# Performance work log

Hardware: AMD Instinct MI355X
Metric: run time of the kernel (lower is better)

The kernel has to match this reference:

```python
import jax, jax.numpy as jnp
import numpy as np

N, E, G = 100000, 500000, 1000


def _gat(h_in, src, dst, W, a_s, a_d, b, n):
    # PyG GATConv, heads=1, concat=True, negative_slope=0.2, self-loops already in src/dst
    h = h_in @ W.T                                  # [N, out]
    alpha_src = h @ a_s                             # [N]
    alpha_dst = h @ a_d                             # [N]
    e = jax.nn.leaky_relu(alpha_src[src] + alpha_dst[dst], 0.2)  # [E']
    m = jax.ops.segment_max(e, dst, num_segments=n)
    ex = jnp.exp(e - m[dst])
    den = jax.ops.segment_sum(ex, dst, num_segments=n)
    alpha = ex / den[dst]                           # segment softmax over incoming edges
    out = jax.ops.segment_sum(h[src] * alpha[:, None], dst, num_segments=n)
    return out + b


def _forward(x, edge_index, batch, w1, b1, w2, b2, w3, b3,
             g1w, g1as, g1ad, g1b, g2w, g2as, g2ad, g2b,
             g3w, g3as, g3ad, g3b, g4w, g4as, g4ad, g4b,
             g5w, g5as, g5ad, g5b, lw, lb):
    n = x.shape[0]
    h = jax.nn.relu(x @ w1.T + b1)
    h = jax.nn.relu(h @ w2.T + b2)
    h = jax.nn.relu(h @ w3.T + b3)
    loops = jnp.arange(n)
    src = jnp.concatenate([edge_index[0], loops])   # add self-loops
    dst = jnp.concatenate([edge_index[1], loops])
    h = jax.nn.relu(_gat(h, src, dst, g1w, g1as, g1ad, g1b, n))
    h = jax.nn.relu(_gat(h, src, dst, g2w, g2as, g2ad, g2b, n))
    h = jax.nn.relu(_gat(h, src, dst, g3w, g3as, g3ad, g3b, n))
    h = jax.nn.relu(_gat(h, src, dst, g4w, g4as, g4ad, g4b, n))
    h = jax.nn.relu(_gat(h, src, dst, g5w, g5as, g5ad, g5b, n))
    sums = jax.ops.segment_sum(h, batch, num_segments=G)            # [G,32]
    cnt = jax.ops.segment_sum(jnp.ones((n,), h.dtype), batch, num_segments=G)
    mean = sums / jnp.maximum(cnt, 1.0)[:, None]
    return jax.nn.sigmoid(mean @ lw.T + lb)         # [G,1]


def setup_inputs() -> dict:
    key = jax.random.key(0)
    ks = jax.random.split(key, 24)

    def lin(k, o, i):
        k1, k2 = jax.random.split(k)
        s = 1.0 / np.sqrt(i)
        return (jax.random.uniform(k1, (o, i), jnp.float32, -s, s),
                jax.random.uniform(k2, (o,), jnp.float32, -s, s))

    def gat_p(k, i, o):
        k1, k2, k3 = jax.random.split(k, 3)
        s = 1.0 / np.sqrt(i)
        W = jax.random.uniform(k1, (o, i), jnp.float32, -s, s)
        a_s = jax.random.normal(k2, (o,), jnp.float32) / np.sqrt(o)
        a_d = jax.random.normal(k3, (o,), jnp.float32) / np.sqrt(o)
        return W, a_s, a_d, jnp.zeros((o,), jnp.float32)

    inp = {}
    inp['x'] = jax.random.normal(ks[0], (N, 1), jnp.float32)
    inp['edge_index'] = jax.random.randint(ks[1], (2, E), 0, N)
    inp['batch'] = jnp.sort(jax.random.randint(ks[2], (N,), 0, G))
    inp['w1'], inp['b1'] = lin(ks[3], 16, 1)
    inp['w2'], inp['b2'] = lin(ks[4], 32, 16)
    inp['w3'], inp['b3'] = lin(ks[5], 64, 32)
    dims = [(64, 128), (128, 256), (256, 128), (128, 64), (64, 32)]
    for j, (i, o) in enumerate(dims, start=1):
        W, a_s, a_d, b = gat_p(ks[5 + j], i, o)
        inp[f'g{j}w'], inp[f'g{j}as'], inp[f'g{j}ad'], inp[f'g{j}b'] = W, a_s, a_d, b
    inp['lw'], inp['lb'] = lin(ks[12], 1, 32)
    return inp


def reference(x, edge_index, batch, w1, b1, w2, b2, w3, b3,
              g1w, g1as, g1ad, g1b, g2w, g2as, g2ad, g2b,
              g3w, g3as, g3ad, g3b, g4w, g4as, g4ad, g4b,
              g5w, g5as, g5ad, g5b, lw, lb):
    return _forward(x, edge_index, batch, w1, b1, w2, b2, w3, b3,
                    g1w, g1as, g1ad, g1b, g2w, g2as, g2ad, g2b,
                    g3w, g3as, g3ad, g3b, g4w, g4as, g4ad, g4b,
                    g5w, g5as, g5ad, g5b, lw, lb)
```

## Files before the change

kernel.cpp:

```cpp
#include <hip/hip_runtime.h>
#include <math.h>

typedef __attribute__((ext_vector_type(8))) __bf16 bf16x8;
typedef __attribute__((ext_vector_type(4))) float f32x4;

__device__ inline unsigned short f2bf(float f) {
    unsigned int i = __float_as_uint(f);
    unsigned int r = i + 0x7fffu + ((i >> 16) & 1u);
    return (unsigned short)(r >> 16);
}
__device__ inline float bf2f(unsigned short u) {
    return __uint_as_float(((unsigned int)u) << 16);
}

__global__ __launch_bounds__(256) void prelude_kernel(
    const float* __restrict__ x,
    const float* __restrict__ w1, const float* __restrict__ b1,
    const float* __restrict__ w2, const float* __restrict__ b2,
    const float* __restrict__ w3, const float* __restrict__ b3,
    unsigned short* __restrict__ h0, int n,
    const float* __restrict__ g0, const float* __restrict__ g1, const float* __restrict__ g2,
    const float* __restrict__ g3, const float* __restrict__ g4,
    unsigned short* __restrict__ wbAll,
    const int* __restrict__ batch, int* __restrict__ gstart, int G,
    const int* __restrict__ dst, int* __restrict__ deg, int E,
    int mlpB, int f2bfB, int gsB, int histB,
    const float* __restrict__ as1, const float* __restrict__ ad1,
    float* __restrict__ s1out, float* __restrict__ d1out,
    const float* __restrict__ as2, const float* __restrict__ ad2,
    float* __restrict__ pv2) {
    int b = blockIdx.x;
    int tid = threadIdx.x;
    if (b < mlpB) {
        __shared__ float4 sw1q[4], sb1q[4];
        __shared__ float4 sw2q[128];
        __shared__ float4 sw3q[512];
        __shared__ float2 psd1[64];
        __shared__ float sb2l[32], sb3l[64];
        __shared__ float pres[4][64], predu[4][64];
        {
            int ii = tid & 63, ch = tid >> 6;
            const float* gp = g0 + (size_t)(ch * 32) * 64 + ii;
            float s = 0.f, d = 0.f;
#pragma unroll 4
            for (int o = 0; o < 32; o++) {
                float w = gp[o * 64];
                s += as1[ch * 32 + o] * w;
                d += ad1[ch * 32 + o] * w;
            }
            pres[ch][ii] = s;
            predu[ch][ii] = d;
        }
        if (tid < 4) { sw1q[tid] = ((const float4*)w1)[tid]; sb1q[tid] = ((const float4*)b1)[tid]; }
        if (tid >= 32 && tid < 64) sb2l[tid - 32] = b2[tid - 32];
        if (tid >= 64 && tid < 128) sb3l[tid - 64] = b3[tid - 64];
        for (int i = tid; i < 128; i += 256) sw2q[i] = ((const float4*)w2)[i];
        for (int i = tid; i < 512; i += 256) sw3q[i] = ((const float4*)w3)[i];
        __syncthreads();
        if (tid < 64) {
            psd1[tid] =
                make_float2(pres[0][tid] + pres[1][tid] + pres[2][tid] + pres[3][tid],
                            predu[0][tid] + predu[1][tid] + predu[2][tid] + predu[3][tid]);
        }
        __syncthreads();
        int node = b * 256 + tid;
        if (node >= n) return;
        float xv = x[node];
        float t1[16], t2[32];
#pragma unroll
        for (int q = 0; q < 4; q++) {
            float4 wv = sw1q[q], bv = sb1q[q];
            t1[q * 4 + 0] = fmaxf(wv.x * xv + bv.x, 0.f);
            t1[q * 4 + 1] = fmaxf(wv.y * xv + bv.y, 0.f);
            t1[q * 4 + 2] = fmaxf(wv.z * xv + bv.z, 0.f);
            t1[q * 4 + 3] = fmaxf(wv.w * xv + bv.w, 0.f);
        }
#pragma unroll
        for (int o = 0; o < 32; o++) {
            float a = sb2l[o];
#pragma unroll
            for (int q = 0; q < 4; q++) {
                float4 wv = sw2q[o * 4 + q];
                a += wv.x * t1[q * 4] + wv.y * t1[q * 4 + 1] + wv.z * t1[q * 4 + 2] +
                     wv.w * t1[q * 4 + 3];
            }
            t2[o] = fmaxf(a, 0.f);
        }
        float sdot = 0.f, ddot = 0.f;
        uint4* gp = (uint4*)(h0 + (size_t)node * 64);
#pragma unroll
        for (int c = 0; c < 8; c++) {
            unsigned int wvec[4];
#pragma unroll
            for (int p = 0; p < 4; p++) {
                int o = c * 8 + p * 2;
                float a0 = sb3l[o], a1 = sb3l[o + 1];
#pragma unroll
                for (int q = 0; q < 8; q++) {
                    float4 wa = sw3q[o * 8 + q];
                    float4 wb = sw3q[(o + 1) * 8 + q];
                    a0 += wa.x * t2[q * 4] + wa.y * t2[q * 4 + 1] + wa.z * t2[q * 4 + 2] +
                          wa.w * t2[q * 4 + 3];
                    a1 += wb.x * t2[q * 4] + wb.y * t2[q * 4 + 1] + wb.z * t2[q * 4 + 2] +
                          wb.w * t2[q * 4 + 3];
                }
                float r0 = fmaxf(a0, 0.f), r1 = fmaxf(a1, 0.f);
                float2 q0 = psd1[o], q1 = psd1[o + 1];
                sdot += r0 * q0.x + r1 * q1.x;
                ddot += r0 * q0.y + r1 * q1.y;
                wvec[p] = (unsigned)f2bf(r0) | ((unsigned)f2bf(r1) << 16);
            }
            gp[c] = make_uint4(wvec[0], wvec[1], wvec[2], wvec[3]);
        }
        s1out[node] = sdot;
        d1out[node] = ddot;
    } else if (b < mlpB + f2bfB) {
        int i = (b - mlpB) * 256 + tid;
        float v;
        if (i < 8192) v = g0[i];
        else if (i < 40960) v = g1[i - 8192];
        else if (i < 73728) v = g2[i - 40960];
        else if (i < 81920) v = g3[i - 73728];
        else if (i < 83968) v = g4[i - 81920];
        else return;
        wbAll[i] = f2bf(v);
    } else if (b < mlpB + f2bfB + gsB) {
        int g = (b - mlpB - f2bfB) * 256 + tid;
        if (g > G) return;
        if (g == G) { gstart[G] = n; return; }
        int lo = 0, hi = n;
        while (lo < hi) {
            int mid = (lo + hi) >> 1;
            if (batch[mid] < g) lo = mid + 1;
            else hi = mid;
        }
        gstart[g] = lo;
    } else if (b < mlpB + f2bfB + gsB + histB) {
        int e = (b - mlpB - f2bfB - gsB) * 256 + tid;
        if (e >= E + n) return;
        int d = (e < E) ? dst[e] : (e - E);
        atomicAdd(&deg[d], 1);
    } else {
        if (tid < 128) {
            float s = 0.f;
            for (int o = 0; o < 256; o++) s += as2[o] * g1[o * 128 + tid];
            pv2[tid] = s;
        } else {
            int c = tid - 128;
            float s = 0.f;
            for (int o = 0; o < 256; o++) s += ad2[o] * g1[o * 128 + c];
            pv2[128 + c] = s;
        }
    }
}

template <int BN, int EPI>
__global__ __launch_bounds__(256) void gemm_mfma(
    const unsigned short* __restrict__ A, const unsigned short* __restrict__ Wb,
    unsigned short* __restrict__ Cb,
    const float* __restrict__ avs, const float* __restrict__ avd,
    float* __restrict__ as_, float* __restrict__ ad_,
    const float* __restrict__ bias, int n, int K, int O) {
    constexpr int SN = BN / 32;
    __shared__ unsigned short As[128][72];
    __shared__ unsigned short Ws[BN][72];
    int tid = threadIdx.x;
    int row0 = blockIdx.x * 128, col0 = blockIdx.y * BN;
    int w = tid >> 6, lane = tid & 63;
    int wr = w >> 1, wc = w & 1;
    int quad = lane >> 4, l15 = lane & 15;
    f32x4 acc[4][SN];
#pragma unroll
    for (int mi = 0; mi < 4; mi++)
#pragma unroll
        for (int ni = 0; ni < SN; ni++) acc[mi][ni] = (f32x4){0.f, 0.f, 0.f, 0.f};

    for (int k0 = 0; k0 < K; k0 += 64) {
#pragma unroll
        for (int i = tid; i < 1024; i += 256) {
            int r = i >> 3, c8 = i & 7;
            int gr = row0 + r;
            uint4 v = make_uint4(0u, 0u, 0u, 0u);
            if (gr < n) v = *(const uint4*)(A + (size_t)gr * K + k0 + c8 * 8);
            *(uint4*)&As[r][c8 * 8] = v;
        }
#pragma unroll
        for (int i = tid; i < BN * 8; i += 256) {
            int r = i >> 3, c8 = i & 7;
            uint4 v = *(const uint4*)(Wb + (size_t)(col0 + r) * K + k0 + c8 * 8);
            *(uint4*)&Ws[r][c8 * 8] = v;
        }
        __syncthreads();
#pragma unroll
        for (int kk = 0; kk < 64; kk += 32) {
            bf16x8 bfr[SN];
#pragma unroll
            for (int ni = 0; ni < SN; ni++)
                bfr[ni] = *(const bf16x8*)&Ws[wc * (BN / 2) + ni * 16 + l15][kk + quad * 8];
#pragma unroll
            for (int mi = 0; mi < 4; mi++) {
                bf16x8 afr = *(const bf16x8*)&As[wr * 64 + mi * 16 + l15][kk + quad * 8];
#pragma unroll
                for (int ni = 0; ni < SN; ni++)
                    acc[mi][ni] = __builtin_amdgcn_mfma_f32_16x16x32_bf16(afr, bfr[ni],
                                                                          acc[mi][ni], 0, 0, 0);
            }
        }
        __syncthreads();
    }
    float avsv[SN], avdv[SN], bv[SN];
    int gc[SN];
#pragma unroll
    for (int ni = 0; ni < SN; ni++) {
        gc[ni] = col0 + wc * (BN / 2) + ni * 16 + l15;
        if constexpr (EPI != 2) {
            avsv[ni] = avs[gc[ni]];
            avdv[ni] = avd[gc[ni]];
        }
        if constexpr (EPI >= 1) bv[ni] = bias[gc[ni]];
    }
#pragma unroll
    for (int mi = 0; mi < 4; mi++) {
        int gm0 = row0 + wr * 64 + mi * 16 + quad * 4;
        float ps[4] = {0.f, 0.f, 0.f, 0.f}, pd[4] = {0.f, 0.f, 0.f, 0.f};
#pragma unroll
        for (int ni = 0; ni < SN; ni++) {
#pragma unroll
            for (int r = 0; r < 4; r++) {
                float d = acc[mi][ni][r];
                if constexpr (EPI >= 1) d = fmaxf(d + bv[ni], 0.f);
                int gm = gm0 + r;
                if (gm < n) Cb[(size_t)gm * O + gc[ni]] = f2bf(d);
                if constexpr (EPI != 2) {
                    ps[r] += d * avsv[ni];
                    pd[r] += d * avdv[ni];
                }
            }
        }
        if constexpr (EPI != 2) {
#pragma unroll
            for (int r = 0; r < 4; r++) {
#pragma unroll
                for (int m = 1; m <= 8; m <<= 1) {
                    ps[r] += __shfl_xor(ps[r], m);
                    pd[r] += __shfl_xor(pd[r], m);
                }
            }
            if (l15 == 0) {
#pragma unroll
                for (int r = 0; r < 4; r++) {
                    int gm = gm0 + r;
                    if (gm < n) {
                        atomicAdd(&as_[gm], ps[r]);
                        atomicAdd(&ad_[gm], pd[r]);
                    }
                }
            }
        }
    }
}

__global__ void scan_block_sums(const int* __restrict__ deg, int* __restrict__ bsums, int n) {
    __shared__ int sdata[256];
    int tid = threadIdx.x;
    int base = blockIdx.x * 1024 + tid * 4;
    int s = 0;
    for (int i = 0; i < 4; i++) {
        int g = base + i;
        if (g < n) s += deg[g];
    }
    sdata[tid] = s;
    __syncthreads();
    for (int off = 128; off > 0; off >>= 1) {
        if (tid < off) sdata[tid] += sdata[tid + off];
        __syncthreads();
    }
    if (tid == 0) bsums[blockIdx.x] = sdata[0];
}

__global__ void scan_write(const int* __restrict__ deg, const int* __restrict__ bsums,
                           int* __restrict__ rowptr, int* __restrict__ cursor, int n, int nb) {
    __shared__ int sdata[256];
    int tid = threadIdx.x;
    sdata[tid] = (tid < blockIdx.x && tid < nb) ? bsums[tid] : 0;
    __syncthreads();
    for (int off = 128; off > 0; off >>= 1) {
        if (tid < off) sdata[tid] += sdata[tid + off];
        __syncthreads();
    }
    int base = sdata[0];
    __syncthreads();
    int gbase = blockIdx.x * 1024 + tid * 4;
    int v[4];
    int s = 0;
    for (int i = 0; i < 4; i++) {
        int g = gbase + i;
        v[i] = (g < n) ? deg[g] : 0;
        s += v[i];
    }
    sdata[tid] = s;
    __syncthreads();
    for (int off = 1; off < 256; off <<= 1) {
        int t = (tid >= off) ? sdata[tid - off] : 0;
        __syncthreads();
        sdata[tid] += t;
        __syncthreads();
    }
    int excl = sdata[tid] - s + base;
    for (int i = 0; i < 4; i++) {
        int g = gbase + i;
        if (g < n) { rowptr[g] = excl; cursor[g] = excl; }
        excl += v[i];
    }
    if (blockIdx.x == gridDim.x - 1 && tid == 255) rowptr[n] = base + sdata[255];
}

__global__ void scatter_kernel(const int* __restrict__ esrc_in, const int* __restrict__ edst_in,
                               int* __restrict__ cursor, int* __restrict__ esrc, int E, int n) {
    int e = blockIdx.x * 256 + threadIdx.x;
    if (e >= E + n) return;
    int s, d;
    if (e < E) { s = esrc_in[e]; d = edst_in[e]; }
    else { s = e - E; d = e - E; }
    int pos = atomicAdd(&cursor[d], 1);
    esrc[pos] = s;
}

template <int O, bool BIASRELU>
__global__ __launch_bounds__(256) void gat_aggregate(
    const unsigned short* __restrict__ hl, const float* __restrict__ as_,
    const float* __restrict__ ad_, const int* __restrict__ rowptr,
    const int* __restrict__ esrc, const float* __restrict__ bias,
    unsigned short* __restrict__ hout, int n, float* __restrict__ zeroBuf, int zeroCnt) {
    int gtid = blockIdx.x * 256 + threadIdx.x;
    if (gtid < zeroCnt) zeroBuf[gtid] = 0.f;
    constexpr int C8 = O / 8;
    constexpr int EPP = 16 / C8;
    int tid = threadIdx.x;
    int v = blockIdx.x * 16 + (tid >> 4);
    int l = tid & 15;
    int gbase = tid & 48;
    if (v >= n) return;
    int beg = rowptr[v], end = rowptr[v + 1];
    int deg = end - beg;
    float adv = ad_[v];
    int sub = l / C8;
    int c = l % C8;
    float acc[8] = {0.f, 0.f, 0.f, 0.f, 0.f, 0.f, 0.f, 0.f};
    if (deg <= 16) {
        int sreg = v;
        float e = -1e30f;
        if (l < deg) {
            sreg = esrc[beg + l];
            float t = as_[sreg] + adv;
            e = (t > 0.f) ? t : 0.2f * t;
        }
        float m = e;
#pragma unroll
        for (int o = 8; o > 0; o >>= 1) m = fmaxf(m, __shfl_xor(m, o));
        float ex = (l < deg) ? __expf(e - m) : 0.f;
        float sum = ex;
#pragma unroll
        for (int o = 8; o > 0; o >>= 1) sum += __shfl_xor(sum, o);
        float alpha_r = ex / sum;
        for (int j0 = 0; j0 < deg; j0 += EPP) {
            int idx = j0 + sub;
            int cidx = (idx < deg) ? idx : 0;
            float alpha = __shfl(alpha_r, gbase + cidx);
            int s2 = __shfl(sreg, gbase + cidx);
            if (idx >= deg) alpha = 0.f;
            uint4 raw = ((const uint4*)(hl + (size_t)s2 * O))[c];
            acc[0] += alpha * __uint_as_float(raw.x << 16);
            acc[1] += alpha * __uint_as_float(raw.x & 0xffff0000u);
            acc[2] += alpha * __uint_as_float(raw.y << 16);
            acc[3] += alpha * __uint_as_float(raw.y & 0xffff0000u);
            acc[4] += alpha * __uint_as_float(raw.z << 16);
            acc[5] += alpha * __uint_as_float(raw.z & 0xffff0000u);
            acc[6] += alpha * __uint_as_float(raw.w << 16);
            acc[7] += alpha * __uint_as_float(raw.w & 0xffff0000u);
        }
    } else {
        float mymax = -1e30f;
        for (int j = beg + l; j < end; j += 16) {
            float e = as_[esrc[j]] + adv;
            e = (e > 0.f) ? e : 0.2f * e;
            mymax = fmaxf(mymax, e);
        }
#pragma unroll
        for (int o = 8; o > 0; o >>= 1) mymax = fmaxf(mymax, __shfl_xor(mymax, o));
        float mysum = 0.f;
        for (int j = beg + l; j < end; j += 16) {
            float e = as_[esrc[j]] + adv;
            e = (e > 0.f) ? e : 0.2f * e;
            mysum += __expf(e - mymax);
        }
#pragma unroll
        for (int o = 8; o > 0; o >>= 1) mysum += __shfl_xor(mysum, o);
        float invden = 1.f / mysum;
        for (int j0 = beg; j0 < end; j0 += EPP) {
            int j = j0 + sub;
            bool valid = j < end;
            int s = valid ? esrc[j] : v;
            float e = as_[s] + adv;
            e = (e > 0.f) ? e : 0.2f * e;
            float alpha = valid ? __expf(e - mymax) * invden : 0.f;
            uint4 raw = ((const uint4*)(hl + (size_t)s * O))[c];
            acc[0] += alpha * __uint_as_float(raw.x << 16);
            acc[1] += alpha * __uint_as_float(raw.x & 0xffff0000u);
            acc[2] += alpha * __uint_as_float(raw.y << 16);
            acc[3] += alpha * __uint_as_float(raw.y & 0xffff0000u);
            acc[4] += alpha * __uint_as_float(raw.z << 16);
            acc[5] += alpha * __uint_as_float(raw.z & 0xffff0000u);
            acc[6] += alpha * __uint_as_float(raw.w << 16);
            acc[7] += alpha * __uint_as_float(raw.w & 0xffff0000u);
        }
    }
#pragma unroll
    for (int o = C8; o < 16; o <<= 1)
#pragma unroll
        for (int k = 0; k < 8; k++) acc[k] += __shfl_xor(acc[k], o);
    if (l < C8) {
        unsigned short ov[8];
#pragma unroll
        for (int k = 0; k < 8; k++) {
            float val = acc[k];
            if constexpr (BIASRELU) val = fmaxf(val + bias[c * 8 + k], 0.f);
            ov[k] = f2bf(val);
        }
        uint4 packed;
        packed.x = (unsigned)ov[0] | ((unsigned)ov[1] << 16);
        packed.y = (unsigned)ov[2] | ((unsigned)ov[3] << 16);
        packed.z = (unsigned)ov[4] | ((unsigned)ov[5] << 16);
        packed.w = (unsigned)ov[6] | ((unsigned)ov[7] << 16);
        ((uint4*)(hout + (size_t)v * O))[c] = packed;
    }
}

__global__ __launch_bounds__(256) void pool_final_kernel(
    const unsigned short* __restrict__ h, const int* __restrict__ start,
    const float* __restrict__ lw, const float* __restrict__ lb,
    float* __restrict__ out, int G) {
    __shared__ float red[8][33];
    int g = blockIdx.x;
    if (g >= G) return;
    int beg = start[g], end = start[g + 1];
    int tid = threadIdx.x;
    int nodeLane = tid >> 5, f = tid & 31;
    float acc = 0.f;
    for (int v = beg + nodeLane; v < end; v += 8)
        acc += bf2f(h[(size_t)v * 32 + f]);
    red[nodeLane][f] = acc;
    __syncthreads();
    if (tid < 32) {
        float s = 0.f;
#pragma unroll
        for (int i = 0; i < 8; i++) s += red[i][f];
        float inv = 1.f / fmaxf((float)(end - beg), 1.f);
        float val = s * inv * lw[f];
#pragma unroll
        for (int o = 16; o > 0; o >>= 1) val += __shfl_xor(val, o);
        if (f == 0) out[g] = 1.f / (1.f + __expf(-(val + lb[0])));
    }
}

extern "C" void kernel_launch(void* const* d_in, const int* in_sizes, int n_in,
                              void* d_out, int out_size, void* d_ws, size_t ws_size,
                              hipStream_t stream) {
    const float* x = (const float*)d_in[0];
    const int* ei = (const int*)d_in[1];
    const int* batch = (const int*)d_in[2];
    const float* w1 = (const float*)d_in[3];
    const float* b1 = (const float*)d_in[4];
    const float* w2 = (const float*)d_in[5];
    const float* b2 = (const float*)d_in[6];
    const float* w3 = (const float*)d_in[7];
    const float* b3 = (const float*)d_in[8];
    const float* gw[5];
    const float* gas[5];
    const float* gad[5];
    const float* gb[5];
    for (int l = 0; l < 5; l++) {
        gw[l] = (const float*)d_in[9 + l * 4 + 0];
        gas[l] = (const float*)d_in[9 + l * 4 + 1];
        gad[l] = (const float*)d_in[9 + l * 4 + 2];
        gb[l] = (const float*)d_in[9 + l * 4 + 3];
    }
    const float* lw = (const float*)d_in[29];
    const float* lb = (const float*)d_in[30];
    float* out = (float*)d_out;

    int N = in_sizes[0];
    int E = in_sizes[1] / 2;
    int G = out_size;
    int Etot = E + N;

    char* ws = (char*)d_ws;
    size_t off = 0;
    auto alloc = [&](size_t bytes) -> void* {
        void* p = ws + off;
        off = (off + bytes + 255) & ~(size_t)255;
        return p;
    };
    unsigned short* actA = (unsigned short*)alloc((size_t)N * 256 * 2);
    unsigned short* actB = (unsigned short*)alloc((size_t)N * 256 * 2);
    char* zblock = (char*)alloc((size_t)N * 20);
    float* sd2 = (float*)zblock;
    float* sd3 = sd2 + (size_t)N * 2;
    int* deg = (int*)(zblock + (size_t)N * 16);
    float* sd1 = (float*)alloc((size_t)N * 2 * 4);
    float* pv2 = (float*)alloc(256 * 4);
    int* rowptr = (int*)alloc((size_t)(N + 1) * 4);
    int* cursor = (int*)alloc((size_t)(N + 1) * 4);
    int* esrc = (int*)alloc((size_t)Etot * 4);
    int* bsums = (int*)alloc(4096);
    int* gstart = (int*)alloc((size_t)(G + 1) * 4);
    unsigned short* wbAll = (unsigned short*)alloc((size_t)83968 * 2);
    const int woff[5] = {0, 8192, 40960, 73728, 81920};
    unsigned short* wb[5];
    for (int l = 0; l < 5; l++) wb[l] = wbAll + woff[l];
    (void)ws_size;
    (void)n_in;

    hipMemsetAsync(zblock, 0, (size_t)N * 20, stream);

    int mlpB = (N + 255) / 256;
    int f2bfB = (83968 + 255) / 256;
    int gsB = (G + 1 + 255) / 256;
    int histB = (Etot + 255) / 256;
    prelude_kernel<<<mlpB + f2bfB + gsB + histB + 1, 256, 0, stream>>>(
        x, w1, b1, w2, b2, w3, b3, actA, N, gw[0], gw[1], gw[2], gw[3], gw[4], wbAll, batch,
        gstart, G, ei + E, deg, E, mlpB, f2bfB, gsB, histB,
        gas[0], gad[0], sd1, sd1 + N, gas[1], gad[1], pv2);

    int nb = (N + 1023) / 1024;
    scan_block_sums<<<nb, 256, 0, stream>>>(deg, bsums, N);
    scan_write<<<nb, 256, 0, stream>>>(deg, bsums, rowptr, cursor, N, nb);
    scatter_kernel<<<(Etot + 255) / 256, 256, 0, stream>>>(ei, ei + E, cursor, esrc, E, N);

    int aggBlocks = (N + 15) / 16;
    int gx = (N + 127) / 128;

    gat_aggregate<64, false><<<aggBlocks, 256, 0, stream>>>(
        actA, sd1, sd1 + N, rowptr, esrc, nullptr, actB, N, nullptr, 0);
    {
        dim3 grid(gx, 2);
        gemm_mfma<64, 1><<<grid, 256, 0, stream>>>(actB, wb[0], actA, pv2, pv2 + 128, sd2,
                                                   sd2 + N, gb[0], N, 64, 128);
    }

    gat_aggregate<128, false><<<aggBlocks, 256, 0, stream>>>(
        actA, sd2, sd2 + N, rowptr, esrc, nullptr, actB, N, sd1, 2 * N);
    {
        dim3 grid(gx, 4);
        gemm_mfma<64, 2><<<grid, 256, 0, stream>>>(actB, wb[1], actA, nullptr, nullptr,
                                                   nullptr, nullptr, gb[1], N, 128, 256);
    }

    {
        dim3 grid(gx, 2);
        gemm_mfma<64, 0><<<grid, 256, 0, stream>>>(actA, wb[2], actB, gas[2], gad[2], sd3,
                                                   sd3 + N, nullptr, N, 256, 128);
    }
    gat_aggregate<128, true><<<aggBlocks, 256, 0, stream>>>(
        actB, sd3, sd3 + N, rowptr, esrc, gb[2], actA, N, sd2, 2 * N);

    {
        dim3 grid(gx, 1);
        gemm_mfma<64, 0><<<grid, 256, 0, stream>>>(actA, wb[3], actB, gas[3], gad[3], sd1,
                                                   sd1 + N, nullptr, N, 128, 64);
    }
    gat_aggregate<64, true><<<aggBlocks, 256, 0, stream>>>(
        actB, sd1, sd1 + N, rowptr, esrc, gb[3], actA, N, nullptr, 0);

    {
        dim3 grid(gx, 1);
        gemm_mfma<32, 0><<<grid, 256, 0, stream>>>(actA, wb[4], actB, gas[4], gad[4], sd2,
                                                   sd2 + N, nullptr, N, 64, 32);
    }
    gat_aggregate<32, true><<<aggBlocks, 256, 0, stream>>>(
        actB, sd2, sd2 + N, rowptr, esrc, gb[4], actA, N, nullptr, 0);

    pool_final_kernel<<<G, 256, 0, stream>>>(actA, gstart, lw, lb, out, G);
}
```

Baseline: 463.6 us.

## Split prelude, place self-loops during scan, keep A tile resident across GEMM columns

The prelude kernel is split into a standalone MLP kernel and a misc kernel, removing the per-block branch on the large MLP path. Self-loops are no longer counted by the atomic histogram or scattered. The scan adds one to each degree and writes each node's self-loop directly into the first CSR slot. The GEMM now loads the full-K activation tile into shared memory once and loops over all output column tiles inside the block, instead of launching one block per column tile and reloading A. This cuts global A traffic but reduces grid parallelism and grows shared memory (K up to 256), which may lower occupancy.

```diff
diff --git a/kernel.cpp b/kernel.cpp
--- a/kernel.cpp
+++ b/kernel.cpp
@@ -13,109 +13,112 @@
     return __uint_as_float(((unsigned int)u) << 16);
 }
 
-__global__ __launch_bounds__(256) void prelude_kernel(
+__global__ __launch_bounds__(256) void mlp_kernel(
     const float* __restrict__ x,
     const float* __restrict__ w1, const float* __restrict__ b1,
     const float* __restrict__ w2, const float* __restrict__ b2,
     const float* __restrict__ w3, const float* __restrict__ b3,
     unsigned short* __restrict__ h0, int n,
+    const float* __restrict__ g0,
+    const float* __restrict__ as1, const float* __restrict__ ad1,
+    float* __restrict__ s1out, float* __restrict__ d1out) {
+    int tid = threadIdx.x;
+    __shared__ float4 sw1q[4], sb1q[4];
+    __shared__ float4 sw2q[128];
+    __shared__ float4 sw3q[512];
+    __shared__ float2 psd1[64];
+    __shared__ float sb2l[32], sb3l[64];
+    __shared__ float pres[4][64], predu[4][64];
+    {
+        int ii = tid & 63, ch = tid >> 6;
+        const float* gp = g0 + (size_t)(ch * 32) * 64 + ii;
+        float s = 0.f, d = 0.f;
+#pragma unroll 4
+        for (int o = 0; o < 32; o++) {
+            float w = gp[o * 64];
+            s += as1[ch * 32 + o] * w;
+            d += ad1[ch * 32 + o] * w;
+        }
+        pres[ch][ii] = s;
+        predu[ch][ii] = d;
+    }
+    if (tid < 4) { sw1q[tid] = ((const float4*)w1)[tid]; sb1q[tid] = ((const float4*)b1)[tid]; }
+    if (tid >= 32 && tid < 64) sb2l[tid - 32] = b2[tid - 32];
+    if (tid >= 64 && tid < 128) sb3l[tid - 64] = b3[tid - 64];
+    for (int i = tid; i < 128; i += 256) sw2q[i] = ((const float4*)w2)[i];
+    for (int i = tid; i < 512; i += 256) sw3q[i] = ((const float4*)w3)[i];
+    __syncthreads();
+    if (tid < 64) {
+        psd1[tid] = make_float2(pres[0][tid] + pres[1][tid] + pres[2][tid] + pres[3][tid],
+                                predu[0][tid] + predu[1][tid] + predu[2][tid] + predu[3][tid]);
+    }
+    __syncthreads();
+    int node = blockIdx.x * 256 + tid;
+    if (node >= n) return;
+    float xv = x[node];
+    float t1[16], t2[32];
+#pragma unroll
+    for (int q = 0; q < 4; q++) {
+        float4 wv = sw1q[q], bv = sb1q[q];
+        t1[q * 4 + 0] = fmaxf(wv.x * xv + bv.x, 0.f);
+        t1[q * 4 + 1] = fmaxf(wv.y * xv + bv.y, 0.f);
+        t1[q * 4 + 2] = fmaxf(wv.z * xv + bv.z, 0.f);
+        t1[q * 4 + 3] = fmaxf(wv.w * xv + bv.w, 0.f);
+    }
+#pragma unroll
+    for (int o = 0; o < 32; o++) {
+        float a = sb2l[o];
+#pragma unroll
+        for (int q = 0; q < 4; q++) {
+            float4 wv = sw2q[o * 4 + q];
+            a += wv.x * t1[q * 4] + wv.y * t1[q * 4 + 1] + wv.z * t1[q * 4 + 2] +
+                 wv.w * t1[q * 4 + 3];
+        }
+        t2[o] = fmaxf(a, 0.f);
+    }
+    float sdot = 0.f, ddot = 0.f;
+    uint4* gp = (uint4*)(h0 + (size_t)node * 64);
+#pragma unroll
+    for (int c = 0; c < 8; c++) {
+        unsigned int wvec[4];
+#pragma unroll
+        for (int p = 0; p < 4; p++) {
+            int o = c * 8 + p * 2;
+            float a0 = sb3l[o], a1 = sb3l[o + 1];
+#pragma unroll
+            for (int q = 0; q < 8; q++) {
+                float4 wa = sw3q[o * 8 + q];
+                float4 wb = sw3q[(o + 1) * 8 + q];
+                a0 += wa.x * t2[q * 4] + wa.y * t2[q * 4 + 1] + wa.z * t2[q * 4 + 2] +
+                      wa.w * t2[q * 4 + 3];
+                a1 += wb.x * t2[q * 4] + wb.y * t2[q * 4 + 1] + wb.z * t2[q * 4 + 2] +
+                      wb.w * t2[q * 4 + 3];
+            }
+            float r0 = fmaxf(a0, 0.f), r1 = fmaxf(a1, 0.f);
+            float2 q0 = psd1[o], q1 = psd1[o + 1];
+            sdot += r0 * q0.x + r1 * q1.x;
+            ddot += r0 * q0.y + r1 * q1.y;
+            wvec[p] = (unsigned)f2bf(r0) | ((unsigned)f2bf(r1) << 16);
+        }
+        gp[c] = make_uint4(wvec[0], wvec[1], wvec[2], wvec[3]);
+    }
+    s1out[node] = sdot;
+    d1out[node] = ddot;
+}
+
+__global__ __launch_bounds__(256) void misc_kernel(
     const float* __restrict__ g0, const float* __restrict__ g1, const float* __restrict__ g2,
     const float* __restrict__ g3, const float* __restrict__ g4,
     unsigned short* __restrict__ wbAll,
-    const int* __restrict__ batch, int* __restrict__ gstart, int G,
+    const int* __restrict__ batch, int* __restrict__ gstart, int G, int n,
     const int* __restrict__ dst, int* __restrict__ deg, int E,
-    int mlpB, int f2bfB, int gsB, int histB,
-    const float* __restrict__ as1, const float* __restrict__ ad1,
-    float* __restrict__ s1out, float* __restrict__ d1out,
+    int f2bfB, int gsB, int histB,
     const float* __restrict__ as2, const float* __restrict__ ad2,
     float* __restrict__ pv2) {
     int b = blockIdx.x;
     int tid = threadIdx.x;
-    if (b < mlpB) {
-        __shared__ float4 sw1q[4], sb1q[4];
-        __shared__ float4 sw2q[128];
-        __shared__ float4 sw3q[512];
-        __shared__ float2 psd1[64];
-        __shared__ float sb2l[32], sb3l[64];
-        __shared__ float pres[4][64], predu[4][64];
-        {
-            int ii = tid & 63, ch = tid >> 6;
-            const float* gp = g0 + (size_t)(ch * 32) * 64 + ii;
-            float s = 0.f, d = 0.f;
-#pragma unroll 4
-            for (int o = 0; o < 32; o++) {
-                float w = gp[o * 64];
-                s += as1[ch * 32 + o] * w;
-                d += ad1[ch * 32 + o] * w;
-            }
-            pres[ch][ii] = s;
-            predu[ch][ii] = d;
-        }
-        if (tid < 4) { sw1q[tid] = ((const float4*)w1)[tid]; sb1q[tid] = ((const float4*)b1)[tid]; }
-        if (tid >= 32 && tid < 64) sb2l[tid - 32] = b2[tid - 32];
-        if (tid >= 64 && tid < 128) sb3l[tid - 64] = b3[tid - 64];
-        for (int i = tid; i < 128; i += 256) sw2q[i] = ((const float4*)w2)[i];
-        for (int i = tid; i < 512; i += 256) sw3q[i] = ((const float4*)w3)[i];
-        __syncthreads();
-        if (tid < 64) {
-            psd1[tid] =
-                make_float2(pres[0][tid] + pres[1][tid] + pres[2][tid] + pres[3][tid],
-                            predu[0][tid] + predu[1][tid] + predu[2][tid] + predu[3][tid]);
-        }
-        __syncthreads();
-        int node = b * 256 + tid;
-        if (node >= n) return;
-        float xv = x[node];
-        float t1[16], t2[32];
-#pragma unroll
-        for (int q = 0; q < 4; q++) {
-            float4 wv = sw1q[q], bv = sb1q[q];
-            t1[q * 4 + 0] = fmaxf(wv.x * xv + bv.x, 0.f);
-            t1[q * 4 + 1] = fmaxf(wv.y * xv + bv.y, 0.f);
-            t1[q * 4 + 2] = fmaxf(wv.z * xv + bv.z, 0.f);
-            t1[q * 4 + 3] = fmaxf(wv.w * xv + bv.w, 0.f);
-        }
-#pragma unroll
-        for (int o = 0; o < 32; o++) {
-            float a = sb2l[o];
-#pragma unroll
-            for (int q = 0; q < 4; q++) {
-                float4 wv = sw2q[o * 4 + q];
-                a += wv.x * t1[q * 4] + wv.y * t1[q * 4 + 1] + wv.z * t1[q * 4 + 2] +
-                     wv.w * t1[q * 4 + 3];
-            }
-            t2[o] = fmaxf(a, 0.f);
-        }
-        float sdot = 0.f, ddot = 0.f;
-        uint4* gp = (uint4*)(h0 + (size_t)node * 64);
-#pragma unroll
-        for (int c = 0; c < 8; c++) {
-            unsigned int wvec[4];
-#pragma unroll
-            for (int p = 0; p < 4; p++) {
-                int o = c * 8 + p * 2;
-                float a0 = sb3l[o], a1 = sb3l[o + 1];
-#pragma unroll
-                for (int q = 0; q < 8; q++) {
-                    float4 wa = sw3q[o * 8 + q];
-                    float4 wb = sw3q[(o + 1) * 8 + q];
-                    a0 += wa.x * t2[q * 4] + wa.y * t2[q * 4 + 1] + wa.z * t2[q * 4 + 2] +
-                          wa.w * t2[q * 4 + 3];
-                    a1 += wb.x * t2[q * 4] + wb.y * t2[q * 4 + 1] + wb.z * t2[q * 4 + 2] +
-                          wb.w * t2[q * 4 + 3];
-                }
-                float r0 = fmaxf(a0, 0.f), r1 = fmaxf(a1, 0.f);
-                float2 q0 = psd1[o], q1 = psd1[o + 1];
-                sdot += r0 * q0.x + r1 * q1.x;
-                ddot += r0 * q0.y + r1 * q1.y;
-                wvec[p] = (unsigned)f2bf(r0) | ((unsigned)f2bf(r1) << 16);
-            }
-            gp[c] = make_uint4(wvec[0], wvec[1], wvec[2], wvec[3]);
-        }
-        s1out[node] = sdot;
-        d1out[node] = ddot;
-    } else if (b < mlpB + f2bfB) {
-        int i = (b - mlpB) * 256 + tid;
+    if (b < f2bfB) {
+        int i = b * 256 + tid;
         float v;
         if (i < 8192) v = g0[i];
         else if (i < 40960) v = g1[i - 8192];
@@ -124,8 +127,8 @@
         else if (i < 83968) v = g4[i - 81920];
         else return;
         wbAll[i] = f2bf(v);
-    } else if (b < mlpB + f2bfB + gsB) {
-        int g = (b - mlpB - f2bfB) * 256 + tid;
+    } else if (b < f2bfB + gsB) {
+        int g = (b - f2bfB) * 256 + tid;
         if (g > G) return;
         if (g == G) { gstart[G] = n; return; }
         int lo = 0, hi = n;
@@ -135,11 +138,10 @@
             else hi = mid;
         }
         gstart[g] = lo;
-    } else if (b < mlpB + f2bfB + gsB + histB) {
-        int e = (b - mlpB - f2bfB - gsB) * 256 + tid;
-        if (e >= E + n) return;
-        int d = (e < E) ? dst[e] : (e - E);
-        atomicAdd(&deg[d], 1);
+    } else if (b < f2bfB + gsB + histB) {
+        int e = (b - f2bfB - gsB) * 256 + tid;
+        if (e >= E) return;
+        atomicAdd(&deg[dst[e]], 1);
     } else {
         if (tid < 128) {
             float s = 0.f;
@@ -154,105 +156,110 @@
     }
 }
 
-template <int BN, int EPI>
+template <int K, int BN, int EPI>
 __global__ __launch_bounds__(256) void gemm_mfma(
     const unsigned short* __restrict__ A, const unsigned short* __restrict__ Wb,
     unsigned short* __restrict__ Cb,
     const float* __restrict__ avs, const float* __restrict__ avd,
     float* __restrict__ as_, float* __restrict__ ad_,
-    const float* __restrict__ bias, int n, int K, int O) {
+    const float* __restrict__ bias, int n, int O) {
     constexpr int SN = BN / 32;
-    __shared__ unsigned short As[128][72];
+    constexpr int K8 = K / 8;
+    __shared__ unsigned short As[128][K + 8];
     __shared__ unsigned short Ws[BN][72];
     int tid = threadIdx.x;
-    int row0 = blockIdx.x * 128, col0 = blockIdx.y * BN;
+    int row0 = blockIdx.x * 128;
     int w = tid >> 6, lane = tid & 63;
     int wr = w >> 1, wc = w & 1;
     int quad = lane >> 4, l15 = lane & 15;
-    f32x4 acc[4][SN];
-#pragma unroll
-    for (int mi = 0; mi < 4; mi++)
-#pragma unroll
-        for (int ni = 0; ni < SN; ni++) acc[mi][ni] = (f32x4){0.f, 0.f, 0.f, 0.f};
-
-    for (int k0 = 0; k0 < K; k0 += 64) {
-#pragma unroll
-        for (int i = tid; i < 1024; i += 256) {
-            int r = i >> 3, c8 = i & 7;
-            int gr = row0 + r;
-            uint4 v = make_uint4(0u, 0u, 0u, 0u);
-            if (gr < n) v = *(const uint4*)(A + (size_t)gr * K + k0 + c8 * 8);
-            *(uint4*)&As[r][c8 * 8] = v;
-        }
-#pragma unroll
-        for (int i = tid; i < BN * 8; i += 256) {
-            int r = i >> 3, c8 = i & 7;
-            uint4 v = *(const uint4*)(Wb + (size_t)(col0 + r) * K + k0 + c8 * 8);
-            *(uint4*)&Ws[r][c8 * 8] = v;
-        }
-        __syncthreads();
-#pragma unroll
-        for (int kk = 0; kk < 64; kk += 32) {
-            bf16x8 bfr[SN];
-#pragma unroll
-            for (int ni = 0; ni < SN; ni++)
-                bfr[ni] = *(const bf16x8*)&Ws[wc * (BN / 2) + ni * 16 + l15][kk + quad * 8];
-#pragma unroll
-            for (int mi = 0; mi < 4; mi++) {
-                bf16x8 afr = *(const bf16x8*)&As[wr * 64 + mi * 16 + l15][kk + quad * 8];
+
+    for (int i = tid; i < 128 * K8; i += 256) {
+        int r = i / K8, c8 = i % K8;
+        int gr = row0 + r;
+        uint4 v = make_uint4(0u, 0u, 0u, 0u);
+        if (gr < n) v = *(const uint4*)(A + (size_t)gr * K + c8 * 8);
+        *(uint4*)&As[r][c8 * 8] = v;
+    }
+
+    for (int ot = 0; ot * BN < O; ot++) {
+        int col0 = ot * BN;
+        f32x4 acc[4][SN];
+#pragma unroll
+        for (int mi = 0; mi < 4; mi++)
+#pragma unroll
+            for (int ni = 0; ni < SN; ni++) acc[mi][ni] = (f32x4){0.f, 0.f, 0.f, 0.f};
+#pragma unroll 1
+        for (int k0 = 0; k0 < K; k0 += 64) {
+#pragma unroll
+            for (int i = tid; i < BN * 8; i += 256) {
+                int r = i >> 3, c8 = i & 7;
+                uint4 v = *(const uint4*)(Wb + (size_t)(col0 + r) * K + k0 + c8 * 8);
+                *(uint4*)&Ws[r][c8 * 8] = v;
+            }
+            __syncthreads();
+#pragma unroll
+            for (int kk = 0; kk < 64; kk += 32) {
+                bf16x8 bfr[SN];
 #pragma unroll
                 for (int ni = 0; ni < SN; ni++)
-                    acc[mi][ni] = __builtin_amdgcn_mfma_f32_16x16x32_bf16(afr, bfr[ni],
-                                                                          acc[mi][ni], 0, 0, 0);
-            }
-        }
-        __syncthreads();
-    }
-    float avsv[SN], avdv[SN], bv[SN];
-    int gc[SN];
-#pragma unroll
-    for (int ni = 0; ni < SN; ni++) {
-        gc[ni] = col0 + wc * (BN / 2) + ni * 16 + l15;
-        if constexpr (EPI != 2) {
-            avsv[ni] = avs[gc[ni]];
-            avdv[ni] = avd[gc[ni]];
-        }
-        if constexpr (EPI >= 1) bv[ni] = bias[gc[ni]];
-    }
-#pragma unroll
-    for (int mi = 0; mi < 4; mi++) {
-        int gm0 = row0 + wr * 64 + mi * 16 + quad * 4;
-        float ps[4] = {0.f, 0.f, 0.f, 0.f}, pd[4] = {0.f, 0.f, 0.f, 0.f};
-#pragma unroll
-        for (int ni = 0; ni < SN; ni++) {
-#pragma unroll
-            for (int r = 0; r < 4; r++) {
-                float d = acc[mi][ni][r];
-                if constexpr (EPI >= 1) d = fmaxf(d + bv[ni], 0.f);
-                int gm = gm0 + r;
-                if (gm < n) Cb[(size_t)gm * O + gc[ni]] = f2bf(d);
-                if constexpr (EPI != 2) {
-                    ps[r] += d * avsv[ni];
-                    pd[r] += d * avdv[ni];
+                    bfr[ni] = *(const bf16x8*)&Ws[wc * (BN / 2) + ni * 16 + l15][kk + quad * 8];
+#pragma unroll
+                for (int mi = 0; mi < 4; mi++) {
+                    bf16x8 afr = *(const bf16x8*)&As[wr * 64 + mi * 16 + l15][k0 + kk + quad * 8];
+#pragma unroll
+                    for (int ni = 0; ni < SN; ni++)
+                        acc[mi][ni] = __builtin_amdgcn_mfma_f32_16x16x32_bf16(
+                            afr, bfr[ni], acc[mi][ni], 0, 0, 0);
                 }
             }
-        }
-        if constexpr (EPI != 2) {
-#pragma unroll
-            for (int r = 0; r < 4; r++) {
-#pragma unroll
-                for (int m = 1; m <= 8; m <<= 1) {
-                    ps[r] += __shfl_xor(ps[r], m);
-                    pd[r] += __shfl_xor(pd[r], m);
+            __syncthreads();
+        }
+        float avsv[SN], avdv[SN], bv[SN];
+        int gc[SN];
+#pragma unroll
+        for (int ni = 0; ni < SN; ni++) {
+            gc[ni] = col0 + wc * (BN / 2) + ni * 16 + l15;
+            if constexpr (EPI != 2) {
+                avsv[ni] = avs[gc[ni]];
+                avdv[ni] = avd[gc[ni]];
+            }
+            if constexpr (EPI >= 1) bv[ni] = bias[gc[ni]];
+        }
+#pragma unroll
+        for (int mi = 0; mi < 4; mi++) {
+            int gm0 = row0 + wr * 64 + mi * 16 + quad * 4;
+            float ps[4] = {0.f, 0.f, 0.f, 0.f}, pd[4] = {0.f, 0.f, 0.f, 0.f};
+#pragma unroll
+            for (int ni = 0; ni < SN; ni++) {
+#pragma unroll
+                for (int r = 0; r < 4; r++) {
+                    float d = acc[mi][ni][r];
+                    if constexpr (EPI >= 1) d = fmaxf(d + bv[ni], 0.f);
+                    int gm = gm0 + r;
+                    if (gm < n) Cb[(size_t)gm * O + gc[ni]] = f2bf(d);
+                    if constexpr (EPI != 2) {
+                        ps[r] += d * avsv[ni];
+                        pd[r] += d * avdv[ni];
+                    }
                 }
             }
-            if (l15 == 0) {
+            if constexpr (EPI != 2) {
 #pragma unroll
                 for (int r = 0; r < 4; r++) {
-                    int gm = gm0 + r;
-                    if (gm < n) {
-                        atomicAdd(&as_[gm], ps[r]);
-                        atomicAdd(&ad_[gm], pd[r]);
+#pragma unroll
+                    for (int m = 1; m <= 8; m <<= 1) {
+                        ps[r] += __shfl_xor(ps[r], m);
+                        pd[r] += __shfl_xor(pd[r], m);
+                    }
+                }
+                if (l15 == 0) {
+#pragma unroll
+                    for (int r = 0; r < 4; r++) {
+                        int gm = gm0 + r;
+                        if (gm < n) {
+                            atomicAdd(&as_[gm], ps[r]);
+                            atomicAdd(&ad_[gm], pd[r]);
+                        }
                     }
                 }
             }
@@ -267,7 +274,7 @@
     int s = 0;
     for (int i = 0; i < 4; i++) {
         int g = base + i;
-        if (g < n) s += deg[g];
+        if (g < n) s += deg[g] + 1;
     }
     sdata[tid] = s;
     __syncthreads();
@@ -279,7 +286,8 @@
 }
 
 __global__ void scan_write(const int* __restrict__ deg, const int* __restrict__ bsums,
-                           int* __restrict__ rowptr, int* __restrict__ cursor, int n, int nb) {
+                           int* __restrict__ rowptr, int* __restrict__ cursor,
+                           int* __restrict__ esrc, int n, int nb) {
     __shared__ int sdata[256];
     int tid = threadIdx.x;
     sdata[tid] = (tid < blockIdx.x && tid < nb) ? bsums[tid] : 0;
@@ -295,7 +303,7 @@
     int s = 0;
     for (int i = 0; i < 4; i++) {
         int g = gbase + i;
-        v[i] = (g < n) ? deg[g] : 0;
+        v[i] = (g < n) ? deg[g] + 1 : 0;
         s += v[i];
     }
     sdata[tid] = s;
@@ -309,21 +317,22 @@
     int excl = sdata[tid] - s + base;
     for (int i = 0; i < 4; i++) {
         int g = gbase + i;
-        if (g < n) { rowptr[g] = excl; cursor[g] = excl; }
+        if (g < n) {
+            rowptr[g] = excl;
+            esrc[excl] = g;
+            cursor[g] = excl + 1;
+        }
         excl += v[i];
     }
     if (blockIdx.x == gridDim.x - 1 && tid == 255) rowptr[n] = base + sdata[255];
 }
 
 __global__ void scatter_kernel(const int* __restrict__ esrc_in, const int* __restrict__ edst_in,
-                               int* __restrict__ cursor, int* __restrict__ esrc, int E, int n) {
+                               int* __restrict__ cursor, int* __restrict__ esrc, int E) {
     int e = blockIdx.x * 256 + threadIdx.x;
-    if (e >= E + n) return;
-    int s, d;
-    if (e < E) { s = esrc_in[e]; d = edst_in[e]; }
-    else { s = e - E; d = e - E; }
-    int pos = atomicAdd(&cursor[d], 1);
-    esrc[pos] = s;
+    if (e >= E) return;
+    int pos = atomicAdd(&cursor[edst_in[e]], 1);
+    esrc[pos] = esrc_in[e];
 }
 
 template <int O, bool BIASRELU>
@@ -523,60 +532,46 @@
 
     hipMemsetAsync(zblock, 0, (size_t)N * 20, stream);
 
-    int mlpB = (N + 255) / 256;
     int f2bfB = (83968 + 255) / 256;
     int gsB = (G + 1 + 255) / 256;
-    int histB = (Etot + 255) / 256;
-    prelude_kernel<<<mlpB + f2bfB + gsB + histB + 1, 256, 0, stream>>>(
-        x, w1, b1, w2, b2, w3, b3, actA, N, gw[0], gw[1], gw[2], gw[3], gw[4], wbAll, batch,
-        gstart, G, ei + E, deg, E, mlpB, f2bfB, gsB, histB,
-        gas[0], gad[0], sd1, sd1 + N, gas[1], gad[1], pv2);
+    int histB = (E + 255) / 256;
+    misc_kernel<<<f2bfB + gsB + histB + 1, 256, 0, stream>>>(
+        gw[0], gw[1], gw[2], gw[3], gw[4], wbAll, batch, gstart, G, N, ei + E, deg, E,
+        f2bfB, gsB, histB, gas[1], gad[1], pv2);
+
+    mlp_kernel<<<(N + 255) / 256, 256, 0, stream>>>(x, w1, b1, w2, b2, w3, b3, actA, N,
+                                                    gw[0], gas[0], gad[0], sd1, sd1 + N);
 
     int nb = (N + 1023) / 1024;
     scan_block_sums<<<nb, 256, 0, stream>>>(deg, bsums, N);
-    scan_write<<<nb, 256, 0, stream>>>(deg, bsums, rowptr, cursor, N, nb);
-    scatter_kernel<<<(Etot + 255) / 256, 256, 0, stream>>>(ei, ei + E, cursor, esrc, E, N);
+    scan_write<<<nb, 256, 0, stream>>>(deg, bsums, rowptr, cursor, esrc, N, nb);
+    scatter_kernel<<<(E + 255) / 256, 256, 0, stream>>>(ei, ei + E, cursor, esrc, E);
 
     int aggBlocks = (N + 15) / 16;
     int gx = (N + 127) / 128;
 
     gat_aggregate<64, false><<<aggBlocks, 256, 0, stream>>>(
         actA, sd1, sd1 + N, rowptr, esrc, nullptr, actB, N, nullptr, 0);
-    {
-        dim3 grid(gx, 2);
-        gemm_mfma<64, 1><<<grid, 256, 0, stream>>>(actB, wb[0], actA, pv2, pv2 + 128, sd2,
-                                                   sd2 + N, gb[0], N, 64, 128);
-    }
+    gemm_mfma<64, 64, 1><<<gx, 256, 0, stream>>>(actB, wb[0], actA, pv2, pv2 + 128, sd2,
+                                                 sd2 + N, gb[0], N, 128);
 
     gat_aggregate<128, false><<<aggBlocks, 256, 0, stream>>>(
         actA, sd2, sd2 + N, rowptr, esrc, nullptr, actB, N, sd1, 2 * N);
-    {
-        dim3 grid(gx, 4);
-        gemm_mfma<64, 2><<<grid, 256, 0, stream>>>(actB, wb[1], actA, nullptr, nullptr,
-                                                   nullptr, nullptr, gb[1], N, 128, 256);
-    }
-
-    {
-        dim3 grid(gx, 2);
-        gemm_mfma<64, 0><<<grid, 256, 0, stream>>>(actA, wb[2], actB, gas[2], gad[2], sd3,
-                                                   sd3 + N, nullptr, N, 256, 128);
-    }
+    gemm_mfma<128, 64, 2><<<gx, 256, 0, stream>>>(actB, wb[1], actA, nullptr, nullptr,
+                                                  nullptr, nullptr, gb[1], N, 256);
+
+    gemm_mfma<256, 64, 0><<<gx, 256, 0, stream>>>(actA, wb[2], actB, gas[2], gad[2], sd3,
+                                                  sd3 + N, nullptr, N, 128);
     gat_aggregate<128, true><<<aggBlocks, 256, 0, stream>>>(
         actB, sd3, sd3 + N, rowptr, esrc, gb[2], actA, N, sd2, 2 * N);
 
-    {
-        dim3 grid(gx, 1);
-        gemm_mfma<64, 0><<<grid, 256, 0, stream>>>(actA, wb[3], actB, gas[3], gad[3], sd1,
-                                                   sd1 + N, nullptr, N, 128, 64);
-    }
+    gemm_mfma<128, 64, 0><<<gx, 256, 0, stream>>>(actA, wb[3], actB, gas[3], gad[3], sd1,
+                                                  sd1 + N, nullptr, N, 64);
     gat_aggregate<64, true><<<aggBlocks, 256, 0, stream>>>(
         actB, sd1, sd1 + N, rowptr, esrc, gb[3], actA, N, nullptr, 0);
 
-    {
-        dim3 grid(gx, 1);
-        gemm_mfma<32, 0><<<grid, 256, 0, stream>>>(actA, wb[4], actB, gas[4], gad[4], sd2,
-                                                   sd2 + N, nullptr, N, 64, 32);
-    }
+    gemm_mfma<64, 32, 0><<<gx, 256, 0, stream>>>(actA, wb[4], actB, gas[4], gad[4], sd2,
+                                                 sd2 + N, nullptr, N, 32);
     gat_aggregate<32, true><<<aggBlocks, 256, 0, stream>>>(
         actB, sd2, sd2 + N, rowptr, esrc, gb[4], actA, N, nullptr, 0);
 
```

Result: slower. 500.9 us (+8.1%).
